# Performance work log

Hardware: AMD Instinct MI355X
Metric: run time of the kernel (lower is better)

Reference implementation:

```python
import jax, jax.numpy as jnp
import numpy as np

N, K, D, V = 20000, 16, 256, 64  # nodes, neighbors, embed_dim, edge vocab


def setup_inputs() -> dict:
    key = jax.random.key(0)
    ks = jax.random.split(key, 16)
    s = 1.0 / np.sqrt(2 * D)  # Linear(512 -> 256) init scale
    return {
        "node_reps": jax.random.normal(ks[0], (1, N, D), jnp.float32),
        "in_indices": jax.random.randint(ks[1], (1, N, K), 0, N, jnp.int32),
        "in_edges": jax.random.randint(ks[2], (1, N, K), 0, V, jnp.int32),
        "in_mask": jax.random.uniform(ks[3], (1, N, K), jnp.float32),
        "out_indices": jax.random.randint(ks[4], (1, N, K), 0, N, jnp.int32),
        "out_edges": jax.random.randint(ks[5], (1, N, K), 0, V, jnp.int32),
        "out_mask": jax.random.uniform(ks[6], (1, N, K), jnp.float32),
        "edge_emb_1": jax.random.normal(ks[7], (V, D), jnp.float32),
        "W_1": jax.random.uniform(ks[8], (2 * D, D), jnp.float32, -s, s),
        "b_1": jnp.zeros((D,), jnp.float32),
        "edge_emb_2": jax.random.normal(ks[9], (V, D), jnp.float32),
        "W_2": jax.random.uniform(ks[10], (2 * D, D), jnp.float32, -s, s),
        "b_2": jnp.zeros((D,), jnp.float32),
        "edge_emb_3": jax.random.normal(ks[11], (V, D), jnp.float32),
        "W_3": jax.random.uniform(ks[12], (2 * D, D), jnp.float32, -s, s),
        "b_3": jnp.zeros((D,), jnp.float32),
    }


def gcn_layer(node_reps, in_idx, in_edg, in_msk, out_idx, out_edg, out_msk,
              edge_emb, W, b):
    # node_reps: [1, N, D]; dropout is identity in eval mode.
    nodes = node_reps[0]  # [N, D]; batch_size == 1 as in the original repo

    def agg(idx, edg, msk):
        nbr = nodes[idx]          # gather: [1, N, K, D]
        erep = edge_emb[edg]      # embedding lookup: [1, N, K, D]
        reps = jnp.concatenate([nbr, erep], axis=3) * msk[..., None]
        return reps.sum(axis=2)   # masked sum over neighbors: [1, N, 2D]

    in_reps = agg(in_idx, in_edg, in_msk)
    out_reps = agg(out_idx, out_edg, out_msk)
    in_nodes = in_reps[0] @ W + b    # [N, D]
    out_nodes = out_reps[0] @ W + b  # [N, D]
    return node_reps + out_nodes + in_nodes  # broadcast -> [1, N, D]


def reference(node_reps, in_indices, in_edges, in_mask,
              out_indices, out_edges, out_mask,
              edge_emb_1, W_1, b_1, edge_emb_2, W_2, b_2, edge_emb_3, W_3, b_3):
    nbrs = (in_indices, in_edges, in_mask, out_indices, out_edges, out_mask)
    hidden = gcn_layer(node_reps, *nbrs, edge_emb_1, W_1, b_1)  # gc1
    mu = gcn_layer(hidden, *nbrs, edge_emb_2, W_2, b_2)          # gc2
    logvar = gcn_layer(hidden, *nbrs, edge_emb_3, W_3, b_3)      # gc3

    mu_t = jnp.tanh(mu[0])        # [N, D]
    lv_t = jnp.tanh(logvar[0])    # [N, D]
    n_nodes = mu_t.shape[0]
    kld = (-0.5 / n_nodes) * jnp.mean(
        jnp.sum(1.0 + 2.0 * lv_t - mu_t ** 2 - jnp.exp(lv_t) ** 2, axis=1))
    return hidden, kld
```

## Files before the change

kernel.cpp:

```cpp
#include <hip/hip_runtime.h>
#include <math.h>

#define NN 20000
#define KK 16
#define DD 256
#define VV 64
#define NT1 16
#define SAS 336
#define SAS8 336

typedef __attribute__((ext_vector_type(8))) __bf16 bf16x8;
typedef __attribute__((ext_vector_type(4))) float floatx4;
typedef __attribute__((ext_vector_type(2))) float floatx2;
typedef __attribute__((ext_vector_type(8))) unsigned short ushort8;
typedef __attribute__((ext_vector_type(4))) unsigned int uint4v;

__device__ __forceinline__ float4 ld4(const float* p) { return *reinterpret_cast<const float4*>(p); }

__device__ __forceinline__ unsigned short f2bf(float f) {
    union { float f; unsigned u; } v; v.f = f;
    unsigned r = v.u + 0x7FFFu + ((v.u >> 16) & 1u);
    return (unsigned short)(r >> 16);
}
__device__ __forceinline__ float bf2f(unsigned short u) {
    union { unsigned u; float f; } v; v.u = ((unsigned)u) << 16;
    return v.f;
}
__device__ __forceinline__ unsigned char f2q(float f) {
    return (unsigned char)(__builtin_amdgcn_cvt_pk_fp8_f32(f, 0.f, 0u, false) & 0xFFu);
}
__device__ __forceinline__ float q2f(unsigned char q) {
    floatx2 r = __builtin_amdgcn_cvt_pk_f32_fp8((unsigned)q, false);
    return r.x;
}
__device__ __forceinline__ float ftanh(float v) {
    float e = __expf(2.f * v);
    return 1.f - 2.f * __builtin_amdgcn_rcpf(e + 1.f);
}

__global__ __launch_bounds__(256) void ewhist(
    const int* __restrict__ ie, const float* __restrict__ im,
    const int* __restrict__ oe, const float* __restrict__ om,
    const float* __restrict__ x,
    const float* __restrict__ e1, const float* __restrict__ W1,
    const float* __restrict__ e2, const float* __restrict__ W2,
    const float* __restrict__ e3, const float* __restrict__ W3,
    float* __restrict__ EW, unsigned short* __restrict__ Hc,
    unsigned short* __restrict__ xh, float* __restrict__ kld) {
    int blk = blockIdx.x, tid = threadIdx.x;
    if (blk < 192) {
        int layer = blk >> 6, v = blk & 63, d = tid;
        const float* emb = layer == 0 ? e1 : (layer == 1 ? e2 : e3);
        const float* W   = layer == 0 ? W1 : (layer == 1 ? W2 : W3);
        float acc = 0.f;
        #pragma unroll 8
        for (int j = 0; j < 256; ++j)
            acc += emb[v * DD + j] * W[(size_t)(256 + j) * DD + d];
        EW[(size_t)layer * VV * DD + v * DD + d] = acc;
    } else {
        int pb = blk - 192;
        int w = tid >> 6, lane = tid & 63;
        int n = pb * 4 + w;
        int e = 0; float m = 0.f;
        if (lane < 16)      { e = ie[n * KK + lane];      m = im[n * KK + lane]; }
        else if (lane < 32) { e = oe[n * KK + lane - 16]; m = om[n * KK + lane - 16]; }
        float h = 0.f;
        #pragma unroll
        for (int j = 0; j < 32; ++j) {
            int ev = __shfl(e, j);
            float mv = __shfl(m, j);
            if (ev == lane) h += mv;
        }
        Hc[(size_t)n * 64 + lane] = f2bf(h);
        size_t base = (size_t)pb * 1024 + tid * 4;
        float4 v = ld4(x + base);
        ushort4 o; o.x = f2bf(v.x); o.y = f2bf(v.y); o.z = f2bf(v.z); o.w = f2bf(v.w);
        *reinterpret_cast<ushort4*>(xh + base) = o;
        if (pb == 0 && tid == 0) *kld = 0.f;
    }
}

__global__ __launch_bounds__(256) void packU(
    const float* __restrict__ W1, const float* __restrict__ W2, const float* __restrict__ W3,
    const float* __restrict__ EW,
    unsigned short* __restrict__ U1, unsigned short* __restrict__ U23) {
    int blk = blockIdx.x, tid = threadIdx.x;
    int u1path = blk < 40;
    int NT = u1path ? 16 : 32;
    int g = (u1path ? blk : blk - 40) * 256 + tid;
    int lane = g & 63, ntk = g >> 6;
    int nt = ntk % NT, kt = ntk / NT;
    if (kt >= 10) return;
    int n = nt * 16 + (lane & 15);
    int kbase = kt * 32 + (lane >> 4) * 8;
    const float* W; const float* EWl;
    if (u1path)       { W = W1; EWl = EW; }
    else if (n < 256) { W = W2; EWl = EW + VV * DD; }
    else              { W = W3; EWl = EW + 2 * VV * DD; n -= 256; }
    unsigned short o8[8];
    #pragma unroll
    for (int j = 0; j < 8; ++j) {
        int k = kbase + j;
        float v = (k < 256) ? W[(size_t)k * DD + n] : EWl[(size_t)(k - 256) * DD + n];
        o8[j] = f2bf(v);
    }
    unsigned short* U = u1path ? U1 : U23;
    *reinterpret_cast<uint4v*>(&U[(size_t)g * 8]) = *reinterpret_cast<uint4v*>(o8);
}

__global__ __launch_bounds__(256) void fmm1(const unsigned short* __restrict__ xh, const unsigned short* __restrict__ Hc,
                                            const int* __restrict__ ii, const float* __restrict__ im,
                                            const int* __restrict__ oi, const float* __restrict__ om,
                                            const unsigned short* __restrict__ U, const float* __restrict__ b,
                                            float* __restrict__ out, unsigned char* __restrict__ h8) {
    __shared__ unsigned short sA[16 * SAS];
    __shared__ int sidx[16][32];
    __shared__ float smsk[16][32];
    int n0 = blockIdx.x * 16;
    int tid = threadIdx.x;
    for (int q = tid; q < 512; q += 256) {
        int r = q >> 5, j = q & 31;
        int n = n0 + r;
        sidx[r][j] = (j < 16) ? ii[n * KK + j] : oi[n * KK + j - 16];
        smsk[r][j] = (j < 16) ? im[n * KK + j] : om[n * KK + j - 16];
    }
    if (tid < 128) {
        int r = tid >> 3, k8 = tid & 7;
        *reinterpret_cast<uint4v*>(&sA[r * SAS + 256 + k8 * 8]) =
            *reinterpret_cast<const uint4v*>(&Hc[(size_t)(n0 + r) * 64 + k8 * 8]);
    }
    __syncthreads();
    int lane = tid & 63, w = tid >> 6;
    int half = lane >> 5, c = (lane & 31) * 8;
    #pragma unroll
    for (int rr = 0; rr < 4; ++rr) {
        int row = w * 4 + rr;
        float acc[8] = {0.f, 0.f, 0.f, 0.f, 0.f, 0.f, 0.f, 0.f};
        #pragma unroll
        for (int j = 0; j < 16; ++j) {
            int j2 = j * 2 + half;
            int idx = sidx[row][j2];
            float m = smsk[row][j2];
            ushort8 u = *reinterpret_cast<const ushort8*>(xh + (size_t)idx * DD + c);
            #pragma unroll
            for (int z = 0; z < 8; ++z) acc[z] += m * bf2f(u[z]);
        }
        #pragma unroll
        for (int z = 0; z < 8; ++z) acc[z] += __shfl_xor(acc[z], 32);
        if (half == 0) {
            unsigned short o8[8];
            #pragma unroll
            for (int z = 0; z < 8; ++z) o8[z] = f2bf(acc[z]);
            *reinterpret_cast<uint4v*>(&sA[row * SAS + c]) = *reinterpret_cast<uint4v*>(o8);
        }
    }
    __syncthreads();
    int lr = lane & 15, quad = lane >> 4;
    float xp[4][4], bb[4];
    #pragma unroll
    for (int t = 0; t < 4; ++t) {
        int col = (w * 4 + t) * 16 + lr;
        bb[t] = 2.f * b[col];
        #pragma unroll
        for (int r = 0; r < 4; ++r)
            xp[t][r] = bf2f(xh[(size_t)(n0 + quad * 4 + r) * DD + col]);
    }
    floatx4 z = {0.f, 0.f, 0.f, 0.f};
    floatx4 acc[4] = {z, z, z, z};
    for (int kt = 0; kt < 10; ++kt) {
        bf16x8 a = *reinterpret_cast<const bf16x8*>(&sA[lr * SAS + kt * 32 + quad * 8]);
        #pragma unroll
        for (int t = 0; t < 4; ++t) {
            bf16x8 bf = *reinterpret_cast<const bf16x8*>(&U[(size_t)((kt * NT1 + w * 4 + t) * 64 + lane) * 8]);
            acc[t] = __builtin_amdgcn_mfma_f32_16x16x32_bf16(a, bf, acc[t], 0, 0, 0);
        }
    }
    #pragma unroll
    for (int t = 0; t < 4; ++t) {
        int col = (w * 4 + t) * 16 + lr;
        #pragma unroll
        for (int r = 0; r < 4; ++r) {
            size_t o = (size_t)(n0 + quad * 4 + r) * DD + col;
            float v = xp[t][r] + bb[t] + acc[t][r];
            out[o] = v;
            h8[o] = f2q(v);
        }
    }
}

__global__ __launch_bounds__(256) void fmm23(const unsigned char* __restrict__ h8, const unsigned short* __restrict__ Hc,
                                             const int* __restrict__ ii, const float* __restrict__ im,
                                             const int* __restrict__ oi, const float* __restrict__ om,
                                             const unsigned short* __restrict__ U, const float* __restrict__ b2,
                                             const float* __restrict__ b3, float* __restrict__ kld) {
    __shared__ unsigned short sA[16 * SAS];
    __shared__ int sidx[16][32];
    __shared__ float smsk[16][32];
    __shared__ float red[4];
    int n0 = blockIdx.x * 16;
    int tid = threadIdx.x;
    for (int q = tid; q < 512; q += 256) {
        int r = q >> 5, j = q & 31;
        int n = n0 + r;
        sidx[r][j] = (j < 16) ? ii[n * KK + j] : oi[n * KK + j - 16];
        smsk[r][j] = (j < 16) ? im[n * KK + j] : om[n * KK + j - 16];
    }
    if (tid < 128) {
        int r = tid >> 3, k8 = tid & 7;
        *reinterpret_cast<uint4v*>(&sA[r * SAS + 256 + k8 * 8]) =
            *reinterpret_cast<const uint4v*>(&Hc[(size_t)(n0 + r) * 64 + k8 * 8]);
    }
    __syncthreads();
    int lane = tid & 63, w = tid >> 6;
    int g = lane >> 4, cl = lane & 15;
    #pragma unroll
    for (int rr = 0; rr < 4; ++rr) {
        int row = w * 4 + rr;
        float acc[16];
        #pragma unroll
        for (int z = 0; z < 16; ++z) acc[z] = 0.f;
        #pragma unroll
        for (int j = 0; j < 8; ++j) {
            int r = g * 8 + j;
            int idx = sidx[row][r];
            float m = smsk[row][r];
            uint4v u = *reinterpret_cast<const uint4v*>(h8 + (size_t)idx * DD + cl * 16);
            #pragma unroll
            for (int d = 0; d < 4; ++d) {
                floatx2 f01 = __builtin_amdgcn_cvt_pk_f32_fp8(u[d], false);
                floatx2 f23 = __builtin_amdgcn_cvt_pk_f32_fp8(u[d], true);
                acc[d * 4 + 0] += m * f01.x; acc[d * 4 + 1] += m * f01.y;
                acc[d * 4 + 2] += m * f23.x; acc[d * 4 + 3] += m * f23.y;
            }
        }
        #pragma unroll
        for (int z = 0; z < 16; ++z) {
            acc[z] += __shfl_xor(acc[z], 16);
            acc[z] += __shfl_xor(acc[z], 32);
        }
        if (g == 0) {
            unsigned short o16[16];
            #pragma unroll
            for (int z = 0; z < 16; ++z) o16[z] = f2bf(acc[z]);
            uint4v* dst = reinterpret_cast<uint4v*>(&sA[row * SAS + cl * 16]);
            dst[0] = reinterpret_cast<uint4v*>(o16)[0];
            dst[1] = reinterpret_cast<uint4v*>(o16)[1];
        }
    }
    __syncthreads();
    int lr = lane & 15, quad = lane >> 4;
    float hp[4][4], bm[4], bl[4];
    #pragma unroll
    for (int t = 0; t < 4; ++t) {
        int col = (w * 4 + t) * 16 + lr;
        bm[t] = 2.f * b2[col];
        bl[t] = 2.f * b3[col];
        #pragma unroll
        for (int r = 0; r < 4; ++r)
            hp[t][r] = q2f(h8[(size_t)(n0 + quad * 4 + r) * DD + col]);
    }
    floatx4 z = {0.f, 0.f, 0.f, 0.f};
    floatx4 am[4] = {z, z, z, z};
    floatx4 al[4] = {z, z, z, z};
    for (int kt = 0; kt < 10; ++kt) {
        bf16x8 a = *reinterpret_cast<const bf16x8*>(&sA[lr * SAS + kt * 32 + quad * 8]);
        #pragma unroll
        for (int t = 0; t < 4; ++t) {
            int nt = w * 4 + t;
            bf16x8 bmu = *reinterpret_cast<const bf16x8*>(&U[(size_t)((kt * 32 + nt) * 64 + lane) * 8]);
            bf16x8 blv = *reinterpret_cast<const bf16x8*>(&U[(size_t)((kt * 32 + 16 + nt) * 64 + lane) * 8]);
            am[t] = __builtin_amdgcn_mfma_f32_16x16x32_bf16(a, bmu, am[t], 0, 0, 0);
            al[t] = __builtin_amdgcn_mfma_f32_16x16x32_bf16(a, blv, al[t], 0, 0, 0);
        }
    }
    float kacc = 0.f;
    #pragma unroll
    for (int t = 0; t < 4; ++t) {
        #pragma unroll
        for (int r = 0; r < 4; ++r) {
            float h = hp[t][r];
            float tm = ftanh(h + bm[t] + am[t][r]);
            float tl = ftanh(h + bl[t] + al[t][r]);
            kacc += (1.f - tm * tm) + (2.f * tl - __expf(2.f * tl));
        }
    }
    #pragma unroll
    for (int off = 32; off > 0; off >>= 1) kacc += __shfl_xor(kacc, off);
    if (lane == 0) red[w] = kacc;
    __syncthreads();
    if (tid == 0)
        atomicAdd(kld, (red[0] + red[1] + red[2] + red[3]) * (-0.5f / ((float)NN * (float)NN)));
}

extern "C" void kernel_launch(void* const* d_in, const int* in_sizes, int n_in,
                              void* d_out, int out_size, void* d_ws, size_t ws_size,
                              hipStream_t stream) {
    const float* x  = (const float*)d_in[0];
    const int*   ii = (const int*)d_in[1];
    const int*   ie = (const int*)d_in[2];
    const float* im = (const float*)d_in[3];
    const int*   oi = (const int*)d_in[4];
    const int*   oe = (const int*)d_in[5];
    const float* om = (const float*)d_in[6];
    const float* e1 = (const float*)d_in[7];
    const float* W1 = (const float*)d_in[8];
    const float* b1 = (const float*)d_in[9];
    const float* e2 = (const float*)d_in[10];
    const float* W2 = (const float*)d_in[11];
    const float* b2 = (const float*)d_in[12];
    const float* e3 = (const float*)d_in[13];
    const float* W3 = (const float*)d_in[14];
    const float* b3 = (const float*)d_in[15];
    float* out = (float*)d_out;
    float* kld = out + (size_t)NN * DD;

    char* ws = (char*)d_ws;
    float*          EW  = (float*)(ws);
    unsigned short* U1  = (unsigned short*)(ws + 196608);
    unsigned short* U23 = (unsigned short*)(ws + 360448);
    unsigned short* Hc  = (unsigned short*)(ws + 688128);
    unsigned short* xh  = (unsigned short*)(ws + 3248128);
    unsigned char*  h8  = (unsigned char*)(ws + 13488128);

    ewhist<<<192 + NN / 4, 256, 0, stream>>>(ie, im, oe, om, x, e1, W1, e2, W2, e3, W3,
                                             EW, Hc, xh, kld);
    packU <<<120, 256, 0, stream>>>(W1, W2, W3, EW, U1, U23);
    fmm1  <<<NN / 16, 256, 0, stream>>>(xh, Hc, ii, im, oi, om, U1, b1, out, h8);
    fmm23 <<<NN / 16, 256, 0, stream>>>(h8, Hc, ii, im, oi, om, U23, b2, b3, kld);
}
```

Before: 192.6 us.

## Split layer-1 neighbor aggregation into a separate gather kernel

The neighbor gather-and-sum for layer 1, which used to run inside the GEMM kernel, becomes its own kernel, agg1. agg1 processes 32 nodes by a quarter of the feature columns per block, with each thread summing all 32 neighbors for 8 columns, and writes bf16 sums to a new workspace buffer. fmm1b then loads those sums into shared memory and runs only the MFMA matmul. The aim is to raise parallelism and memory-level concurrency for the gather and to stop the GEMM from stalling on irregular loads. The cost is an extra launch plus a round trip of a 20000x256 bf16 intermediate through global memory.

```diff
diff --git a/kernel.cpp b/kernel.cpp
--- a/kernel.cpp
+++ b/kernel.cpp
@@ -7,7 +7,6 @@
 #define VV 64
 #define NT1 16
 #define SAS 336
-#define SAS8 336
 
 typedef __attribute__((ext_vector_type(8))) __bf16 bf16x8;
 typedef __attribute__((ext_vector_type(4))) float floatx4;
@@ -108,21 +107,55 @@
     *reinterpret_cast<uint4v*>(&U[(size_t)g * 8]) = *reinterpret_cast<uint4v*>(o8);
 }
 
-__global__ __launch_bounds__(256) void fmm1(const unsigned short* __restrict__ xh, const unsigned short* __restrict__ Hc,
-                                            const int* __restrict__ ii, const float* __restrict__ im,
-                                            const int* __restrict__ oi, const float* __restrict__ om,
-                                            const unsigned short* __restrict__ U, const float* __restrict__ b,
-                                            float* __restrict__ out, unsigned char* __restrict__ h8) {
-    __shared__ unsigned short sA[16 * SAS];
-    __shared__ int sidx[16][32];
-    __shared__ float smsk[16][32];
-    int n0 = blockIdx.x * 16;
+__global__ __launch_bounds__(256) void agg1(
+    const unsigned short* __restrict__ xh,
+    const int* __restrict__ ii, const float* __restrict__ im,
+    const int* __restrict__ oi, const float* __restrict__ om,
+    unsigned short* __restrict__ S) {
+    __shared__ int sidx[32][33];
+    __shared__ float smsk[32][33];
+    int bid = blockIdx.x;
+    int q = bid & 3;
+    int n0 = (bid >> 2) * 32;
     int tid = threadIdx.x;
-    for (int q = tid; q < 512; q += 256) {
-        int r = q >> 5, j = q & 31;
+    for (int p = tid; p < 1024; p += 256) {
+        int r = p >> 5, j = p & 31;
         int n = n0 + r;
         sidx[r][j] = (j < 16) ? ii[n * KK + j] : oi[n * KK + j - 16];
         smsk[r][j] = (j < 16) ? im[n * KK + j] : om[n * KK + j - 16];
+    }
+    __syncthreads();
+    int lane = tid & 63, w = tid >> 6;
+    int row = w * 8 + (lane >> 3);
+    int d0 = q * 64 + (lane & 7) * 8;
+    float acc[8] = {0.f, 0.f, 0.f, 0.f, 0.f, 0.f, 0.f, 0.f};
+    #pragma unroll 8
+    for (int j = 0; j < 32; ++j) {
+        int idx = sidx[row][j];
+        float m = smsk[row][j];
+        ushort8 u = *reinterpret_cast<const ushort8*>(xh + (size_t)idx * DD + d0);
+        #pragma unroll
+        for (int z = 0; z < 8; ++z) acc[z] += m * bf2f(u[z]);
+    }
+    unsigned short o8[8];
+    #pragma unroll
+    for (int z = 0; z < 8; ++z) o8[z] = f2bf(acc[z]);
+    *reinterpret_cast<uint4v*>(&S[(size_t)(n0 + row) * DD + d0]) =
+        *reinterpret_cast<uint4v*>(o8);
+}
+
+__global__ __launch_bounds__(256) void fmm1b(
+    const unsigned short* __restrict__ S, const unsigned short* __restrict__ xh,
+    const unsigned short* __restrict__ Hc,
+    const unsigned short* __restrict__ U, const float* __restrict__ b,
+    float* __restrict__ out, unsigned char* __restrict__ h8) {
+    __shared__ unsigned short sA[16 * SAS];
+    int n0 = blockIdx.x * 16;
+    int tid = threadIdx.x;
+    for (int p = tid; p < 512; p += 256) {
+        int r = p >> 5, c8 = p & 31;
+        *reinterpret_cast<uint4v*>(&sA[r * SAS + c8 * 8]) =
+            *reinterpret_cast<const uint4v*>(&S[(size_t)(n0 + r) * DD + c8 * 8]);
     }
     if (tid < 128) {
         int r = tid >> 3, k8 = tid & 7;
@@ -131,30 +164,6 @@
     }
     __syncthreads();
     int lane = tid & 63, w = tid >> 6;
-    int half = lane >> 5, c = (lane & 31) * 8;
-    #pragma unroll
-    for (int rr = 0; rr < 4; ++rr) {
-        int row = w * 4 + rr;
-        float acc[8] = {0.f, 0.f, 0.f, 0.f, 0.f, 0.f, 0.f, 0.f};
-        #pragma unroll
-        for (int j = 0; j < 16; ++j) {
-            int j2 = j * 2 + half;
-            int idx = sidx[row][j2];
-            float m = smsk[row][j2];
-            ushort8 u = *reinterpret_cast<const ushort8*>(xh + (size_t)idx * DD + c);
-            #pragma unroll
-            for (int z = 0; z < 8; ++z) acc[z] += m * bf2f(u[z]);
-        }
-        #pragma unroll
-        for (int z = 0; z < 8; ++z) acc[z] += __shfl_xor(acc[z], 32);
-        if (half == 0) {
-            unsigned short o8[8];
-            #pragma unroll
-            for (int z = 0; z < 8; ++z) o8[z] = f2bf(acc[z]);
-            *reinterpret_cast<uint4v*>(&sA[row * SAS + c]) = *reinterpret_cast<uint4v*>(o8);
-        }
-    }
-    __syncthreads();
     int lr = lane & 15, quad = lane >> 4;
     float xp[4][4], bb[4];
     #pragma unroll
@@ -321,10 +330,12 @@
     unsigned short* Hc  = (unsigned short*)(ws + 688128);
     unsigned short* xh  = (unsigned short*)(ws + 3248128);
     unsigned char*  h8  = (unsigned char*)(ws + 13488128);
+    unsigned short* S   = (unsigned short*)(ws + 18608128);
 
     ewhist<<<192 + NN / 4, 256, 0, stream>>>(ie, im, oe, om, x, e1, W1, e2, W2, e3, W3,
                                              EW, Hc, xh, kld);
     packU <<<120, 256, 0, stream>>>(W1, W2, W3, EW, U1, U23);
-    fmm1  <<<NN / 16, 256, 0, stream>>>(xh, Hc, ii, im, oi, om, U1, b1, out, h8);
+    agg1  <<<(NN / 32) * 4, 256, 0, stream>>>(xh, ii, im, oi, om, S);
+    fmm1b <<<NN / 16, 256, 0, stream>>>(S, xh, Hc, U1, b1, out, h8);
     fmm23 <<<NN / 16, 256, 0, stream>>>(h8, Hc, ii, im, oi, om, U23, b2, b3, kld);
 }
```

Measured after the change: 195.0 us. No clear change (+1.3%).
